# Kernel optimization log

Measured on AMD Instinct MI355X. Metric: run time of the kernel, lower is better.

## Reference

```python
import jax, jax.numpy as jnp
import numpy as np

NUM_HEADS = 16


def setup_inputs() -> dict:
    key = jax.random.key(0)
    k1, k2, k3 = jax.random.split(key, 3)
    S, B, H = 2048, 2, 1024
    hidden_states = jax.random.normal(k1, (S, B, H), dtype=jnp.float32)
    attention_mask = jnp.zeros((1, S, S), dtype=jnp.float32)
    W_qkv = jax.random.normal(k2, (3 * H, H), dtype=jnp.float32) * 0.02
    b_qkv = jax.random.normal(k3, (3 * H,), dtype=jnp.float32) * 0.02
    return {"hidden_states": hidden_states, "attention_mask": attention_mask,
            "W_qkv": W_qkv, "b_qkv": b_qkv}


def reference(hidden_states, attention_mask, W_qkv, b_qkv):
    # hidden_states: [S, B, H] (seq-first, megatron layout)
    S, B, H = hidden_states.shape
    nh = NUM_HEADS
    hph = H // nh
    norm_factor = jax.lax.rsqrt(jnp.float32(hph))

    # fused QKV projection: [S, B, 3H] -> [S, B, nh, 3*hph]
    qkv = hidden_states @ W_qkv.T + b_qkv
    qkv = qkv.reshape(S, B, nh, 3 * hph)
    q, k, v = jnp.split(qkv, 3, axis=3)  # each [S, B, nh, hph]

    # raw scores: (Q K^T) * rsqrt(hph), megatron layout [B*nh, Sq, Sk]
    scores = jnp.einsum('sbhd,tbhd->bhst', q, k) * norm_factor
    matmul_result = scores.reshape(B * nh, S, S)

    # exp-based unnormalized attention: exp(scores + additive mask), no softmax divide
    attention_probs = jnp.exp(matmul_result + attention_mask)  # [B*nh, S, S]

    # context: probs @ V -> [S, B, nh, hph] -> [S, B, H]
    probs_bh = attention_probs.reshape(B, nh, S, S)
    context = jnp.einsum('bhst,tbhd->sbhd', probs_bh, v)
    context_layer = context.reshape(S, B, H)
    return (context_layer, matmul_result, attention_probs)
```

## Files before the change

### kernel.cpp

```cpp
#include <hip/hip_runtime.h>
#include <hip/hip_bf16.h>

#define S_  2048
#define B_  2
#define H_  1024
#define NH_ 16
#define D_  64

typedef short s16x8 __attribute__((ext_vector_type(8)));
typedef float f32x4 __attribute__((ext_vector_type(4)));
typedef unsigned short u16;

__device__ __forceinline__ u16 f2bf(float f) {
    __hip_bfloat16 h = __float2bfloat16(f);
    union { __hip_bfloat16 h; u16 u; } c; c.h = h; return c.u;
}

#define GLOAD_LDS16(g, l) __builtin_amdgcn_global_load_lds( \
    (const __attribute__((address_space(1))) void*)(g),     \
    (__attribute__((address_space(3))) void*)(l), 16, 0, 0)

__global__ __launch_bounds__(256) void qkv_gemm(
    const float* __restrict__ A, const float* __restrict__ W,
    const float* __restrict__ bias,
    u16* __restrict__ Qb, u16* __restrict__ Kb, u16* __restrict__ Vt)
{
    __shared__ u16 As[128 * 64];
    __shared__ u16 Bs[128 * 64];

    const int tid  = threadIdx.x;
    const int lane = tid & 63;
    const int w    = tid >> 6;
    const int wm   = (w >> 1) * 64;
    const int wn   = (w & 1) * 64;
    const int l15  = lane & 15;
    const int lg   = lane >> 4;
    const int mBase = blockIdx.y * 128;
    const int nBase = blockIdx.x * 128;

    f32x4 acc[4][4] = {};

    for (int kt = 0; kt < 1024; kt += 64) {
        __syncthreads();
        #pragma unroll
        for (int i = 0; i < 8; ++i) {
            int chunk = tid + i * 256;
            int row = chunk >> 4, c4 = chunk & 15;
            float4 av = *(const float4*)(A + (size_t)(mBase + row) * 1024 + kt + c4 * 4);
            float4 bv = *(const float4*)(W + (size_t)(nBase + row) * 1024 + kt + c4 * 4);
            int byte = (row * 128 + c4 * 8) ^ ((row & 7) << 4);
            ushort4 ap; ap.x = f2bf(av.x); ap.y = f2bf(av.y); ap.z = f2bf(av.z); ap.w = f2bf(av.w);
            ushort4 bp; bp.x = f2bf(bv.x); bp.y = f2bf(bv.y); bp.z = f2bf(bv.z); bp.w = f2bf(bv.w);
            *(ushort4*)((char*)As + byte) = ap;
            *(ushort4*)((char*)Bs + byte) = bp;
        }
        __syncthreads();

        #pragma unroll
        for (int kk = 0; kk < 2; ++kk) {
            s16x8 af[4], bfr[4];
            #pragma unroll
            for (int mi = 0; mi < 4; ++mi) {
                int row = wm + mi * 16 + l15;
                int byte = (row * 128 + ((kk * 64 + lg * 16) ^ ((row & 7) << 4)));
                af[mi] = *(const s16x8*)((const char*)As + byte);
            }
            #pragma unroll
            for (int ni = 0; ni < 4; ++ni) {
                int row = wn + ni * 16 + l15;
                int byte = (row * 128 + ((kk * 64 + lg * 16) ^ ((row & 7) << 4)));
                bfr[ni] = *(const s16x8*)((const char*)Bs + byte);
            }
            #pragma unroll
            for (int mi = 0; mi < 4; ++mi)
                #pragma unroll
                for (int ni = 0; ni < 4; ++ni)
                    acc[mi][ni] = __builtin_amdgcn_mfma_f32_16x16x32_bf16(
                        af[mi], bfr[ni], acc[mi][ni], 0, 0, 0);
        }
    }

    #pragma unroll
    for (int ni = 0; ni < 4; ++ni) {
        int gn = nBase + wn + ni * 16 + l15;
        float bv = bias[gn];
        int h  = gn / 192;
        int r  = gn - h * 192;
        int c  = r >> 6;
        int dd = r & 63;
        #pragma unroll
        for (int mi = 0; mi < 4; ++mi) {
            #pragma unroll
            for (int j = 0; j < 4; ++j) {
                int m = mBase + wm + mi * 16 + lg * 4 + j;
                float val = acc[mi][ni][j] + bv;
                int s = m >> 1, b = m & 1;
                int bh = b * 16 + h;
                u16 o = f2bf(val);
                if (c == 0)      Qb[((size_t)bh * S_ + s) * 64 + dd] = o;
                else if (c == 1) Kb[((size_t)bh * S_ + s) * 64 + dd] = o;
                else             Vt[((size_t)bh * 64 + dd) * S_ + s] = o;
            }
        }
    }
}

__global__ __launch_bounds__(256, 3) void attn(
    const u16* __restrict__ Qb, const u16* __restrict__ Kb, const u16* __restrict__ Vt,
    const float* __restrict__ mask,
    float* __restrict__ ctx, float* __restrict__ scores, float* __restrict__ probs)
{
    __shared__ u16 Ks[2][64 * 64];
    __shared__ u16 Vs[2][64 * 64];
    __shared__ u16 Ps[4][16 * 40];
    __shared__ float SG[4][512];

    const int tid  = threadIdx.x;
    const int lane = tid & 63;
    const int w    = tid >> 6;
    const int l15  = lane & 15;
    const int lg   = lane >> 4;

    const int lin  = blockIdx.y * 32 + blockIdx.x;
    const int orig = (lin & 7) * 128 + (lin >> 3);
    const int bh   = orig >> 5;
    const int rowQ = (orig & 31) * 64 + w * 16;

    const int nK = (w * 2) * 64 + lane;
    const int rK0 = nK >> 3, cK0 = (nK & 7) ^ (rK0 & 7);
    const int nK1 = nK + 64;
    const int rK1 = nK1 >> 3, cK1 = (nK1 & 7) ^ (rK1 & 7);

    s16x8 qf[2];
    #pragma unroll
    for (int kk = 0; kk < 2; ++kk)
        qf[kk] = *(const s16x8*)(Qb + ((size_t)bh * S_ + rowQ + l15) * 64 + kk * 32 + lg * 8);

    f32x4 cacc[4] = {};

    auto stage = [&](int buf, int tt) {
        const u16* kbase = Kb + (size_t)bh * S_ * 64 + (size_t)tt * 64;
        const u16* vbase = Vt + (size_t)bh * 64 * S_ + tt;
        GLOAD_LDS16(kbase + (size_t)rK0 * 64 + cK0 * 8, &Ks[buf][(w * 2 + 0) * 512]);
        GLOAD_LDS16(kbase + (size_t)rK1 * 64 + cK1 * 8, &Ks[buf][(w * 2 + 1) * 512]);
        GLOAD_LDS16(vbase + (size_t)rK0 * S_ + cK0 * 8, &Vs[buf][(w * 2 + 0) * 512]);
        GLOAD_LDS16(vbase + (size_t)rK1 * S_ + cK1 * 8, &Vs[buf][(w * 2 + 1) * 512]);
    };

    stage(0, 0);
    __syncthreads();
    int cur = 0;

    const int q = rowQ + l15;
    const float* mrow = mask + (size_t)q * S_;

    const int rdq   = lane >> 3;
    const int rslot = lane & 7;

    for (int tt = 0; tt < S_; tt += 64) {
        if (tt + 64 < S_) stage(cur ^ 1, tt + 64);

        f32x4 mv[4];
        #pragma unroll
        for (int tb = 0; tb < 4; ++tb)
            mv[tb] = *(const f32x4*)(mrow + tt + tb * 16 + lg * 4);

        f32x4 sacc[4] = {};
        #pragma unroll
        for (int kk = 0; kk < 2; ++kk) {
            #pragma unroll
            for (int tb = 0; tb < 4; ++tb) {
                int row = tb * 16 + l15;
                int byte = (row * 128 + ((kk * 64 + lg * 16) ^ ((row & 7) << 4)));
                s16x8 kf = *(const s16x8*)((const char*)Ks[cur] + byte);
                sacc[tb] = __builtin_amdgcn_mfma_f32_16x16x32_bf16(
                    kf, qf[kk], sacc[tb], 0, 0, 0);
            }
        }

        #pragma unroll
        for (int kv = 0; kv < 2; ++kv) {
            f32x4 s4[2], p4[2];
            #pragma unroll
            for (int th = 0; th < 2; ++th) {
                int tb = kv * 2 + th;
                f32x4 sc = sacc[tb];
                s4[th][0] = sc[0] * 0.125f + mv[tb][0];
                s4[th][1] = sc[1] * 0.125f + mv[tb][1];
                s4[th][2] = sc[2] * 0.125f + mv[tb][2];
                s4[th][3] = sc[3] * 0.125f + mv[tb][3];
                int sbyte = l15 * 128 + (((th * 4 + lg) * 16) ^ ((l15 & 7) << 4));
                *(f32x4*)((char*)SG[w] + sbyte) = s4[th];
            }
            #pragma unroll
            for (int p = 0; p < 2; ++p) {
                int qq = p * 8 + rdq;
                int rbyte = qq * 128 + ((rslot * 16) ^ ((qq & 7) << 4));
                f32x4 v = *(const f32x4*)((const char*)SG[w] + rbyte);
                __builtin_nontemporal_store(v, (f32x4*)(scores +
                    (size_t)bh * S_ * S_ + (size_t)(rowQ + qq) * S_ + tt + kv * 32 + rslot * 4));
            }
            #pragma unroll
            for (int th = 0; th < 2; ++th) {
                p4[th][0] = __expf(s4[th][0]); p4[th][1] = __expf(s4[th][1]);
                p4[th][2] = __expf(s4[th][2]); p4[th][3] = __expf(s4[th][3]);
                int sbyte = l15 * 128 + (((th * 4 + lg) * 16) ^ ((l15 & 7) << 4));
                *(f32x4*)((char*)SG[w] + sbyte) = p4[th];
                ushort4 pb;
                pb.x = f2bf(p4[th][0]); pb.y = f2bf(p4[th][1]);
                pb.z = f2bf(p4[th][2]); pb.w = f2bf(p4[th][3]);
                *(ushort4*)((char*)Ps[w] + l15 * 80 + th * 32 + lg * 8) = pb;
            }
            #pragma unroll
            for (int p = 0; p < 2; ++p) {
                int qq = p * 8 + rdq;
                int rbyte = qq * 128 + ((rslot * 16) ^ ((qq & 7) << 4));
                f32x4 v = *(const f32x4*)((const char*)SG[w] + rbyte);
                __builtin_nontemporal_store(v, (f32x4*)(probs +
                    (size_t)bh * S_ * S_ + (size_t)(rowQ + qq) * S_ + tt + kv * 32 + rslot * 4));
            }
            s16x8 pa = *(const s16x8*)((const char*)Ps[w] + l15 * 80 + lg * 16);
            #pragma unroll
            for (int db = 0; db < 4; ++db) {
                int row = db * 16 + l15;
                int byte = (row * 128 + ((kv * 64 + lg * 16) ^ ((row & 7) << 4)));
                s16x8 vb = *(const s16x8*)((const char*)Vs[cur] + byte);
                cacc[db] = __builtin_amdgcn_mfma_f32_16x16x32_bf16(
                    pa, vb, cacc[db], 0, 0, 0);
            }
        }

        asm volatile("s_waitcnt vmcnt(8) lgkmcnt(0)" ::: "memory");
        __builtin_amdgcn_s_barrier();
        cur ^= 1;
    }

    const int b = bh >> 4, h = bh & 15;
    #pragma unroll
    for (int db = 0; db < 4; ++db)
        #pragma unroll
        for (int j = 0; j < 4; ++j) {
            int srow = rowQ + lg * 4 + j;
            int dd = db * 16 + l15;
            __builtin_nontemporal_store(cacc[db][j],
                ctx + ((size_t)srow * B_ + b) * H_ + h * 64 + dd);
        }
}

extern "C" void kernel_launch(void* const* d_in, const int* in_sizes, int n_in,
                              void* d_out, int out_size, void* d_ws, size_t ws_size,
                              hipStream_t stream) {
    const float* hidden = (const float*)d_in[0];
    const float* mask   = (const float*)d_in[1];
    const float* W      = (const float*)d_in[2];
    const float* bias   = (const float*)d_in[3];

    u16* Qb = (u16*)d_ws;
    u16* Kb = Qb + 4194304;
    u16* Vt = Kb + 4194304;

    float* out    = (float*)d_out;
    float* ctx    = out;
    float* scores = out + 4194304;
    float* probs  = out + 138412032;

    qkv_gemm<<<dim3(24, 32), 256, 0, stream>>>(hidden, W, bias, Qb, Kb, Vt);
    attn<<<dim3(32, 32), 256, 0, stream>>>(Qb, Kb, Vt, mask, ctx, scores, probs);
}
```

Measured before the change: 306.3 us.

## Pre-cast QKV inputs to bf16 and reuse fp32 probs tile for PV operand

```diff
diff --git a/kernel.cpp b/kernel.cpp
--- a/kernel.cpp
+++ b/kernel.cpp
@@ -20,8 +20,24 @@
     (const __attribute__((address_space(1))) void*)(g),     \
     (__attribute__((address_space(3))) void*)(l), 16, 0, 0)
 
+__global__ __launch_bounds__(256) void cast_bf16(
+    const float* __restrict__ A, const float* __restrict__ W,
+    u16* __restrict__ Ab, u16* __restrict__ Wb)
+{
+    size_t g = (size_t)blockIdx.x * 256 + threadIdx.x;
+    const float* src; u16* dst;
+    if (g < 524288) { src = A + g * 8; dst = Ab + g * 8; }
+    else            { size_t h = g - 524288; src = W + h * 8; dst = Wb + h * 8; }
+    f32x4 a = *(const f32x4*)src;
+    f32x4 b = *(const f32x4*)(src + 4);
+    ushort4 lo, hi;
+    lo.x = f2bf(a[0]); lo.y = f2bf(a[1]); lo.z = f2bf(a[2]); lo.w = f2bf(a[3]);
+    hi.x = f2bf(b[0]); hi.y = f2bf(b[1]); hi.z = f2bf(b[2]); hi.w = f2bf(b[3]);
+    *(ushort4*)dst = lo; *(ushort4*)(dst + 4) = hi;
+}
+
 __global__ __launch_bounds__(256) void qkv_gemm(
-    const float* __restrict__ A, const float* __restrict__ W,
+    const u16* __restrict__ Ab, const u16* __restrict__ Wb,
     const float* __restrict__ bias,
     u16* __restrict__ Qb, u16* __restrict__ Kb, u16* __restrict__ Vt)
 {
@@ -38,21 +54,24 @@
     const int mBase = blockIdx.y * 128;
     const int nBase = blockIdx.x * 128;
 
+    int rS[4], cS[4];
+    #pragma unroll
+    for (int i = 0; i < 4; ++i) {
+        int n = (w * 4 + i) * 64 + lane;
+        rS[i] = n >> 3;
+        cS[i] = (n & 7) ^ (rS[i] & 7);
+    }
+
     f32x4 acc[4][4] = {};
 
     for (int kt = 0; kt < 1024; kt += 64) {
         __syncthreads();
-        #pragma unroll
-        for (int i = 0; i < 8; ++i) {
-            int chunk = tid + i * 256;
-            int row = chunk >> 4, c4 = chunk & 15;
-            float4 av = *(const float4*)(A + (size_t)(mBase + row) * 1024 + kt + c4 * 4);
-            float4 bv = *(const float4*)(W + (size_t)(nBase + row) * 1024 + kt + c4 * 4);
-            int byte = (row * 128 + c4 * 8) ^ ((row & 7) << 4);
-            ushort4 ap; ap.x = f2bf(av.x); ap.y = f2bf(av.y); ap.z = f2bf(av.z); ap.w = f2bf(av.w);
-            ushort4 bp; bp.x = f2bf(bv.x); bp.y = f2bf(bv.y); bp.z = f2bf(bv.z); bp.w = f2bf(bv.w);
-            *(ushort4*)((char*)As + byte) = ap;
-            *(ushort4*)((char*)Bs + byte) = bp;
+        const u16* ab = Ab + (size_t)mBase * 1024 + kt;
+        const u16* wb = Wb + (size_t)nBase * 1024 + kt;
+        #pragma unroll
+        for (int i = 0; i < 4; ++i) {
+            GLOAD_LDS16(ab + (size_t)rS[i] * 1024 + cS[i] * 8, As + (w * 4 + i) * 512);
+            GLOAD_LDS16(wb + (size_t)rS[i] * 1024 + cS[i] * 8, Bs + (w * 4 + i) * 512);
         }
         __syncthreads();
 
@@ -105,14 +124,13 @@
     }
 }
 
-__global__ __launch_bounds__(256, 3) void attn(
+__global__ __launch_bounds__(256, 4) void attn(
     const u16* __restrict__ Qb, const u16* __restrict__ Kb, const u16* __restrict__ Vt,
     const float* __restrict__ mask,
     float* __restrict__ ctx, float* __restrict__ scores, float* __restrict__ probs)
 {
     __shared__ u16 Ks[2][64 * 64];
     __shared__ u16 Vs[2][64 * 64];
-    __shared__ u16 Ps[4][16 * 40];
     __shared__ float SG[4][512];
 
     const int tid  = threadIdx.x;
@@ -156,6 +174,9 @@
 
     const int rdq   = lane >> 3;
     const int rslot = lane & 7;
+    const int s0 = (lg >> 1) * 4 + (lg & 1) * 2;
+    const int pvbyteA = l15 * 128 + (((s0 + 0) * 16) ^ ((l15 & 7) << 4));
+    const int pvbyteB = l15 * 128 + (((s0 + 1) * 16) ^ ((l15 & 7) << 4));
 
     for (int tt = 0; tt < S_; tt += 64) {
         if (tt + 64 < S_) stage(cur ^ 1, tt + 64);
@@ -206,10 +227,6 @@
                 p4[th][2] = __expf(s4[th][2]); p4[th][3] = __expf(s4[th][3]);
                 int sbyte = l15 * 128 + (((th * 4 + lg) * 16) ^ ((l15 & 7) << 4));
                 *(f32x4*)((char*)SG[w] + sbyte) = p4[th];
-                ushort4 pb;
-                pb.x = f2bf(p4[th][0]); pb.y = f2bf(p4[th][1]);
-                pb.z = f2bf(p4[th][2]); pb.w = f2bf(p4[th][3]);
-                *(ushort4*)((char*)Ps[w] + l15 * 80 + th * 32 + lg * 8) = pb;
             }
             #pragma unroll
             for (int p = 0; p < 2; ++p) {
@@ -219,7 +236,16 @@
                 __builtin_nontemporal_store(v, (f32x4*)(probs +
                     (size_t)bh * S_ * S_ + (size_t)(rowQ + qq) * S_ + tt + kv * 32 + rslot * 4));
             }
-            s16x8 pa = *(const s16x8*)((const char*)Ps[w] + l15 * 80 + lg * 16);
+            f32x4 ra = *(const f32x4*)((const char*)SG[w] + pvbyteA);
+            f32x4 rb = *(const f32x4*)((const char*)SG[w] + pvbyteB);
+            unsigned int w0, w1, w2, w3;
+            asm("v_cvt_pk_bf16_f32 %0, %1, %2" : "=v"(w0) : "v"(ra[0]), "v"(ra[1]));
+            asm("v_cvt_pk_bf16_f32 %0, %1, %2" : "=v"(w1) : "v"(ra[2]), "v"(ra[3]));
+            asm("v_cvt_pk_bf16_f32 %0, %1, %2" : "=v"(w2) : "v"(rb[0]), "v"(rb[1]));
+            asm("v_cvt_pk_bf16_f32 %0, %1, %2" : "=v"(w3) : "v"(rb[2]), "v"(rb[3]));
+            union { unsigned int u[4]; s16x8 v; } pk;
+            pk.u[0] = w0; pk.u[1] = w1; pk.u[2] = w2; pk.u[3] = w3;
+            s16x8 pa = pk.v;
             #pragma unroll
             for (int db = 0; db < 4; ++db) {
                 int row = db * 16 + l15;
@@ -264,6 +290,10 @@
     float* scores = out + 4194304;
     float* probs  = out + 138412032;
 
-    qkv_gemm<<<dim3(24, 32), 256, 0, stream>>>(hidden, W, bias, Qb, Kb, Vt);
+    u16* Ab = (u16*)scores;
+    u16* Wb = Ab + 4194304;
+
+    cast_bf16<<<dim3(3584), 256, 0, stream>>>(hidden, W, Ab, Wb);
+    qkv_gemm<<<dim3(24, 32), 256, 0, stream>>>(Ab, Wb, bias, Qb, Kb, Vt);
     attn<<<dim3(32, 32), 256, 0, stream>>>(Qb, Kb, Vt, mask, ctx, scores, probs);
 }
```

New measurement: 298.1 us. -2.7%, faster.
